# Performance work log

Hardware: AMD Instinct MI355X
Metric: run time of the kernel (lower is better)

## Reference

```python
import jax, jax.numpy as jnp
import numpy as np

NUM_HEADS = 16
HEAD_DIM = 64  # hidden_size / num_heads


def setup_inputs() -> dict:
    key = jax.random.key(0)
    ks = jax.random.split(key, 20)
    B, S, H, K = 16, 1024, 1024, 64
    d = {"hidden_states": jax.random.normal(ks[0], (B, S, H), jnp.float32)}
    i = 1
    for p in ("q", "k", "v", "o"):
        d["W" + p] = jax.random.normal(ks[i], (H, H), jnp.float32) * (1.0 / np.sqrt(H)); i += 1
        d["b" + p] = jax.random.normal(ks[i], (H,), jnp.float32) * 0.02; i += 1
        d["LM" + p] = jax.random.normal(ks[i], (H, K), jnp.float32) * (1.0 / np.sqrt(K)); i += 1
        d["RM" + p] = jax.random.normal(ks[i], (K, H), jnp.float32) * (1.0 / np.sqrt(H)); i += 1
        d["F" + p] = jnp.ones((H,), jnp.float32)
    d["task"] = 0
    return d


def _proj(x, W, b, LM, RM, F):
    # RG weight reconstruction: weight = LM @ RM + W  (task==0 branch)
    w = LM @ RM + W  # [h_out, h_in]
    y = jnp.einsum("bsi,oi->bso", x, w) + b
    return y * F  # SFG per-channel scaling


def reference(hidden_states, Wq, bq, LMq, RMq, Fq, Wk, bk, LMk, RMk, Fk,
              Wv, bv, LMv, RMv, Fv, Wo, bo, LMo, RMo, Fo, task):
    B, S, H = hidden_states.shape
    nh, hd = NUM_HEADS, HEAD_DIM
    q = _proj(hidden_states, Wq, bq, LMq, RMq, Fq).reshape(B, S, nh, hd)
    k = _proj(hidden_states, Wk, bk, LMk, RMk, Fk).reshape(B, S, nh, hd)
    v = _proj(hidden_states, Wv, bv, LMv, RMv, Fv).reshape(B, S, nh, hd)
    scores = jnp.einsum("bqhd,bkhd->bhqk", q, k) / np.sqrt(hd).astype(np.float32)
    probs = jax.nn.softmax(scores, axis=-1)  # attn_dropout rate = 0.0
    ctx = jnp.einsum("bhqk,bkhd->bqhd", probs, v).reshape(B, S, H)
    out = _proj(ctx, Wo, bo, LMo, RMo, Fo)  # proj_dropout rate = 0.0
    return out
```

## Files before the change

### kernel.cpp

```cpp
#include <hip/hip_runtime.h>
#include <cstdint>
#include <cstddef>

typedef short short8 __attribute__((ext_vector_type(8)));
typedef float f32x4 __attribute__((ext_vector_type(4)));
typedef unsigned short us4 __attribute__((ext_vector_type(4)));
typedef unsigned int u32x2 __attribute__((ext_vector_type(2)));

__device__ __forceinline__ unsigned short f2bf(float f) {
  unsigned int u = __float_as_uint(f);
  unsigned int r = (u + 0x7fffu + ((u >> 16) & 1u)) >> 16;
  return (unsigned short)r;
}
__device__ __forceinline__ float exp2_fast(float x) {
  return __builtin_amdgcn_exp2f(x);
}
__device__ __forceinline__ unsigned int cvt_pk_bf16(float a, float b) {
  unsigned int d;
  asm("v_cvt_pk_bf16_f32 %0, %1, %2" : "=v"(d) : "v"(a), "v"(b));
  return d;
}
__device__ __forceinline__ void gload_lds16(const void* g, void* l) {
  auto gp = reinterpret_cast<const __attribute__((address_space(1))) char*>(
      reinterpret_cast<uintptr_t>(g));
  auto lp = reinterpret_cast<__attribute__((address_space(3))) char*>(
      reinterpret_cast<uintptr_t>(l));
  __builtin_amdgcn_global_load_lds(gp, lp, 16, 0, 0);
}

__global__ __launch_bounds__(256) void prep_weights(
    const float* __restrict__ W, const float* __restrict__ bias,
    const float* __restrict__ LM, const float* __restrict__ RM,
    const float* __restrict__ F, float scale,
    unsigned short* __restrict__ Wout, float* __restrict__ bout) {
  const int o = blockIdx.x;
  const int tid = threadIdx.x;
  __shared__ float lm[64];
  if (tid < 64) lm[tid] = LM[o * 64 + tid];
  __syncthreads();
  const float f = F[o] * scale;
#pragma unroll
  for (int j = 0; j < 4; ++j) {
    const int i = tid + j * 256;
    float acc = W[o * 1024 + i];
#pragma unroll 16
    for (int k = 0; k < 64; ++k) acc = fmaf(lm[k], RM[k * 1024 + i], acc);
    Wout[o * 1024 + i] = f2bf(acc * f);
  }
  if (tid == 0) bout[o] = bias[o] * f;
}

__global__ __launch_bounds__(256) void cast_x(const float* __restrict__ x,
                                              unsigned short* __restrict__ y, int n4) {
  const int i = blockIdx.x * 256 + threadIdx.x;
  if (i >= n4) return;
  f32x4 v = *(const f32x4*)(x + (size_t)i * 4);
  us4 o;
  o[0] = f2bf(v[0]); o[1] = f2bf(v[1]); o[2] = f2bf(v[2]); o[3] = f2bf(v[3]);
  *(us4*)(y + (size_t)i * 4) = o;
}

template <int MODE>
__global__ __launch_bounds__(256) void gemm_bt(const unsigned short* __restrict__ A,
                                               const unsigned short* __restrict__ Bw,
                                               const float* __restrict__ bias,
                                               void* __restrict__ Cout,
                                               int M, int N, int K) {
  __shared__ unsigned short sA[128 * 64];
  __shared__ unsigned short sB[128 * 64];
  const int tid = threadIdx.x;
  const int w = tid >> 6;
  const int lane = tid & 63;
  const int quad = lane >> 4;
  const int ln = lane & 15;
  const int bm = blockIdx.x, bn = blockIdx.y;
  const int wm = w >> 1, wn = w & 1;

  f32x4 acc[4][4];
#pragma unroll
  for (int a = 0; a < 4; ++a)
#pragma unroll
    for (int b = 0; b < 4; ++b) acc[a][b] = (f32x4){0.f, 0.f, 0.f, 0.f};

  const size_t Kb = (size_t)K * 2;
  const char* Agb = (const char*)A + (size_t)bm * 128 * Kb;
  const char* Bgb = (const char*)Bw + (size_t)bn * 128 * Kb;
  char* sAb = (char*)sA;
  char* sBb = (char*)sB;
  const int sw = ln & 7;

  for (int k0 = 0; k0 < K; k0 += 64) {
    __syncthreads();
#pragma unroll
    for (int i = 0; i < 4; ++i) {
      const int Lb = w * 4096 + i * 1024 + lane * 16;
      const int r = Lb >> 7;
      const int c = (Lb >> 4) & 7;
      const int cb = ((c ^ (r & 7)) * 16);
      gload_lds16(Agb + (size_t)r * Kb + (size_t)k0 * 2 + cb, sAb + Lb);
      gload_lds16(Bgb + (size_t)r * Kb + (size_t)k0 * 2 + cb, sBb + Lb);
    }
    __syncthreads();
#pragma unroll
    for (int kk = 0; kk < 2; ++kk) {
      short8 af[4], bfv[4];
#pragma unroll
      for (int t = 0; t < 4; ++t) {
        const int ch = ((kk * 4 + quad) ^ sw) * 16;
        af[t]  = *(const short8*)(sAb + (wm * 64 + t * 16 + ln) * 128 + ch);
        bfv[t] = *(const short8*)(sBb + (wn * 64 + t * 16 + ln) * 128 + ch);
      }
#pragma unroll
      for (int mt = 0; mt < 4; ++mt)
#pragma unroll
        for (int nt = 0; nt < 4; ++nt)
          acc[mt][nt] = __builtin_amdgcn_mfma_f32_16x16x32_bf16(af[mt], bfv[nt], acc[mt][nt], 0, 0, 0);
    }
  }

  if (MODE == 0) {
    unsigned short* out = (unsigned short*)Cout;
#pragma unroll
    for (int mt = 0; mt < 4; ++mt) {
#pragma unroll
      for (int nt = 0; nt < 4; ++nt) {
        const int gn = bn * 128 + wn * 64 + nt * 16 + ln;
        const float bv = bias[gn];
        const int pidx = gn >> 10, rem = gn & 1023;
        const int hh = rem >> 6, dd = rem & 63;
        const int gm0 = bm * 128 + wm * 64 + mt * 16 + quad * 4;
        const int bb = gm0 >> 10, ss0 = gm0 & 1023;
        if (pidx < 2) {
#pragma unroll
          for (int r = 0; r < 4; ++r) {
            const size_t off = ((((size_t)pidx * 16 + bb) * 16 + hh) * 1024 + (ss0 + r)) * 64 + dd;
            out[off] = f2bf(acc[mt][nt][r] + bv);
          }
        } else {
          us4 pk;
#pragma unroll
          for (int r = 0; r < 4; ++r) pk[r] = f2bf(acc[mt][nt][r] + bv);
          const size_t off = (size_t)2 * 16777216 +
                             (((size_t)(bb * 16 + hh) * 64 + dd) * 1024 + ss0);
          *(us4*)(out + off) = pk;
        }
      }
    }
  } else {
    float* out = (float*)Cout;
#pragma unroll
    for (int mt = 0; mt < 4; ++mt) {
#pragma unroll
      for (int nt = 0; nt < 4; ++nt) {
        const int gn = bn * 128 + wn * 64 + nt * 16 + ln;
        const float bv = bias[gn];
#pragma unroll
        for (int r = 0; r < 4; ++r) {
          const int gm = bm * 128 + wm * 64 + mt * 16 + quad * 4 + r;
          out[(size_t)gm * N + gn] = acc[mt][nt][r] + bv;
        }
      }
    }
  }
}

__global__ __launch_bounds__(256) void attn(const unsigned short* __restrict__ Qb,
                                            const unsigned short* __restrict__ Kb_,
                                            const unsigned short* __restrict__ VTb,
                                            unsigned short* __restrict__ ctx) {
  __shared__ unsigned short sK[64 * 64];
  __shared__ unsigned short sVT[64 * 64];
  __shared__ unsigned short sP[64 * 72];
  const int tid = threadIdx.x;
  const int w = tid >> 6, lane = tid & 63, quad = lane >> 4, ln = lane & 15;
  const int qt = blockIdx.x, bh = blockIdx.y;
  const int b = bh >> 4, h = bh & 15;

  char* sKb = (char*)sK;
  char* sVb = (char*)sVT;
  char* sPb = (char*)sP;
  const int sw = ln & 7;

  const unsigned short* Qg = Qb + ((size_t)bh * 1024 + (size_t)qt * 64 + w * 16 + ln) * 64;
  const short8 bq0 = *(const short8*)(Qg + quad * 8);
  const short8 bq1 = *(const short8*)(Qg + 32 + quad * 8);

  f32x4 accO[4];
#pragma unroll
  for (int nt = 0; nt < 4; ++nt) accO[nt] = (f32x4){0.f, 0.f, 0.f, 0.f};
  float mrun = -3e38f, lrun = 0.f;

  for (int kt = 0; kt < 16; ++kt) {
    __syncthreads();
    const char* Kg = (const char*)(Kb_ + ((size_t)bh * 1024 + (size_t)kt * 64) * 64);
    const char* Vg = (const char*)(VTb + (size_t)bh * 65536 + (size_t)kt * 64);
#pragma unroll
    for (int i = 0; i < 2; ++i) {
      const int Lb = w * 2048 + i * 1024 + lane * 16;
      const int r = Lb >> 7;
      const int c = (Lb >> 4) & 7;
      const int cb = ((c ^ (r & 7)) * 16);
      gload_lds16(Kg + (size_t)r * 128 + cb, sKb + Lb);
      gload_lds16(Vg + (size_t)r * 2048 + cb, sVb + Lb);
    }
    __syncthreads();

    f32x4 accS[4];
#pragma unroll
    for (int mt = 0; mt < 4; ++mt) accS[mt] = (f32x4){0.f, 0.f, 0.f, 0.f};
#pragma unroll
    for (int mt = 0; mt < 4; ++mt) {
      const short8 ak0 = *(const short8*)(sKb + (mt * 16 + ln) * 128 + (quad ^ sw) * 16);
      accS[mt] = __builtin_amdgcn_mfma_f32_16x16x32_bf16(ak0, bq0, accS[mt], 0, 0, 0);
    }
#pragma unroll
    for (int mt = 0; mt < 4; ++mt) {
      const short8 ak1 = *(const short8*)(sKb + (mt * 16 + ln) * 128 + ((4 + quad) ^ sw) * 16);
      accS[mt] = __builtin_amdgcn_mfma_f32_16x16x32_bf16(ak1, bq1, accS[mt], 0, 0, 0);
    }

    float tmax = -3e38f;
#pragma unroll
    for (int mt = 0; mt < 4; ++mt)
#pragma unroll
      for (int r = 0; r < 4; ++r) tmax = fmaxf(tmax, accS[mt][r]);
    tmax = fmaxf(tmax, __shfl_xor(tmax, 16));
    tmax = fmaxf(tmax, __shfl_xor(tmax, 32));
    const float mnew = fmaxf(mrun, tmax);
    const float alpha = exp2_fast(mrun - mnew);
    mrun = mnew;
    float psum = 0.f;
#pragma unroll
    for (int mt = 0; mt < 4; ++mt) {
      float p0 = exp2_fast(accS[mt][0] - mnew);
      float p1 = exp2_fast(accS[mt][1] - mnew);
      float p2 = exp2_fast(accS[mt][2] - mnew);
      float p3 = exp2_fast(accS[mt][3] - mnew);
      psum += (p0 + p1) + (p2 + p3);
      u32x2 pk;
      pk[0] = cvt_pk_bf16(p0, p1);
      pk[1] = cvt_pk_bf16(p2, p3);
      *(u32x2*)(sP + (w * 16 + ln) * 72 + mt * 16 + quad * 4) = pk;
    }
    psum += __shfl_xor(psum, 16);
    psum += __shfl_xor(psum, 32);
    lrun = lrun * alpha + psum;
#pragma unroll
    for (int r = 0; r < 4; ++r) {
      const float ar = __shfl(alpha, quad * 4 + r);
#pragma unroll
      for (int nt = 0; nt < 4; ++nt) accO[nt][r] *= ar;
    }

#pragma unroll
    for (int kk = 0; kk < 2; ++kk) {
      const short8 ap = *(const short8*)(sPb + (w * 16 + ln) * 144 + kk * 64 + quad * 16);
#pragma unroll
      for (int nt = 0; nt < 4; ++nt) {
        const short8 bv = *(const short8*)(sVb + (nt * 16 + ln) * 128 + ((kk * 4 + quad) ^ sw) * 16);
        accO[nt] = __builtin_amdgcn_mfma_f32_16x16x32_bf16(ap, bv, accO[nt], 0, 0, 0);
      }
    }
  }

  const float inv = 1.0f / lrun;
#pragma unroll
  for (int r = 0; r < 4; ++r) {
    const float ivr = __shfl(inv, quad * 4 + r);
    const int s = qt * 64 + w * 16 + quad * 4 + r;
#pragma unroll
    for (int nt = 0; nt < 4; ++nt) {
      const int d = nt * 16 + ln;
      ctx[((size_t)(b * 1024 + s)) * 1024 + h * 64 + d] = f2bf(accO[nt][r] * ivr);
    }
  }
}

extern "C" void kernel_launch(void* const* d_in, const int* in_sizes, int n_in,
                              void* d_out, int out_size, void* d_ws, size_t ws_size,
                              hipStream_t stream) {
  const float* hs  = (const float*)d_in[0];
  const float* Wq  = (const float*)d_in[1];
  const float* bq  = (const float*)d_in[2];
  const float* LMq = (const float*)d_in[3];
  const float* RMq = (const float*)d_in[4];
  const float* Fq  = (const float*)d_in[5];
  const float* Wk  = (const float*)d_in[6];
  const float* bk  = (const float*)d_in[7];
  const float* LMk = (const float*)d_in[8];
  const float* RMk = (const float*)d_in[9];
  const float* Fk  = (const float*)d_in[10];
  const float* Wv  = (const float*)d_in[11];
  const float* bv  = (const float*)d_in[12];
  const float* LMv = (const float*)d_in[13];
  const float* RMv = (const float*)d_in[14];
  const float* Fv  = (const float*)d_in[15];
  const float* Wo  = (const float*)d_in[16];
  const float* bo  = (const float*)d_in[17];
  const float* LMo = (const float*)d_in[18];
  const float* RMo = (const float*)d_in[19];
  const float* Fo  = (const float*)d_in[20];

  char* p = (char*)d_ws;
  unsigned short* xbf  = (unsigned short*)p; p += (size_t)16384 * 1024 * 2;
  unsigned short* Wqkv = (unsigned short*)p; p += (size_t)3072 * 1024 * 2;
  unsigned short* Wob  = (unsigned short*)p; p += (size_t)1024 * 1024 * 2;
  float* bqkv = (float*)p; p += 3072 * 4;
  float* bob  = (float*)p; p += 1024 * 4;
  unsigned short* qkv = (unsigned short*)p; p += (size_t)3 * 16777216 * 2;
  unsigned short* ctx = (unsigned short*)p; p += (size_t)16777216 * 2;

  const float qscale = 0.125f * 1.4426950408889634f;

  cast_x<<<16384, 256, 0, stream>>>(hs, xbf, 16777216 / 4);
  prep_weights<<<1024, 256, 0, stream>>>(Wq, bq, LMq, RMq, Fq, qscale, Wqkv, bqkv);
  prep_weights<<<1024, 256, 0, stream>>>(Wk, bk, LMk, RMk, Fk, 1.0f, Wqkv + 1024 * 1024, bqkv + 1024);
  prep_weights<<<1024, 256, 0, stream>>>(Wv, bv, LMv, RMv, Fv, 1.0f, Wqkv + 2 * 1024 * 1024, bqkv + 2048);
  prep_weights<<<1024, 256, 0, stream>>>(Wo, bo, LMo, RMo, Fo, 1.0f, Wob, bob);

  gemm_bt<0><<<dim3(128, 24), 256, 0, stream>>>(xbf, Wqkv, bqkv, (void*)qkv, 16384, 3072, 1024);

  attn<<<dim3(16, 256), 256, 0, stream>>>(qkv, qkv + 16777216, qkv + 2 * 16777216, ctx);

  gemm_bt<1><<<dim3(128, 8), 256, 0, stream>>>(ctx, Wob, bob, d_out, 16384, 1024, 1024);
}
```

Before: 522.2 us.

## Process 128 queries per attention block and remap blocks across XCDs

Each wave now handles two 16-row query subtiles, so every K/V tile loaded into shared memory serves 128 queries instead of 64. This halves global K/V traffic and the number of barrier-separated load phases per query, and reuses each K/V fragment read from LDS across two MFMAs. The grid is flattened and block IDs are remapped so that all query tiles of one (batch, head) land on the same XCD, aiming to improve L2 reuse of K/V. The cost is more registers per thread, a larger sP buffer and half as many blocks.

```diff
diff --git a/kernel.cpp b/kernel.cpp
--- a/kernel.cpp
+++ b/kernel.cpp
@@ -5,7 +5,6 @@
 typedef short short8 __attribute__((ext_vector_type(8)));
 typedef float f32x4 __attribute__((ext_vector_type(4)));
 typedef unsigned short us4 __attribute__((ext_vector_type(4)));
-typedef unsigned int u32x2 __attribute__((ext_vector_type(2)));
 
 __device__ __forceinline__ unsigned short f2bf(float f) {
   unsigned int u = __float_as_uint(f);
@@ -170,10 +169,12 @@
                                             unsigned short* __restrict__ ctx) {
   __shared__ unsigned short sK[64 * 64];
   __shared__ unsigned short sVT[64 * 64];
-  __shared__ unsigned short sP[64 * 72];
+  __shared__ unsigned short sP[128 * 72];
   const int tid = threadIdx.x;
   const int w = tid >> 6, lane = tid & 63, quad = lane >> 4, ln = lane & 15;
-  const int qt = blockIdx.x, bh = blockIdx.y;
+  const int bid = blockIdx.x;
+  const int xcd = bid & 7, qt = (bid >> 3) & 7, sbh = bid >> 6;
+  const int bh = xcd * 32 + sbh;
   const int b = bh >> 4, h = bh & 15;
 
   char* sKb = (char*)sK;
@@ -181,14 +182,21 @@
   char* sPb = (char*)sP;
   const int sw = ln & 7;
 
-  const unsigned short* Qg = Qb + ((size_t)bh * 1024 + (size_t)qt * 64 + w * 16 + ln) * 64;
-  const short8 bq0 = *(const short8*)(Qg + quad * 8);
-  const short8 bq1 = *(const short8*)(Qg + 32 + quad * 8);
-
-  f32x4 accO[4];
-#pragma unroll
-  for (int nt = 0; nt < 4; ++nt) accO[nt] = (f32x4){0.f, 0.f, 0.f, 0.f};
-  float mrun = -3e38f, lrun = 0.f;
+  short8 bq[2][2];
+#pragma unroll
+  for (int s = 0; s < 2; ++s) {
+    const unsigned short* Qg =
+        Qb + ((size_t)bh * 1024 + (size_t)qt * 128 + w * 32 + s * 16 + ln) * 64;
+    bq[s][0] = *(const short8*)(Qg + quad * 8);
+    bq[s][1] = *(const short8*)(Qg + 32 + quad * 8);
+  }
+
+  f32x4 accO[2][4];
+#pragma unroll
+  for (int s = 0; s < 2; ++s)
+#pragma unroll
+    for (int nt = 0; nt < 4; ++nt) accO[s][nt] = (f32x4){0.f, 0.f, 0.f, 0.f};
+  float mrun[2] = {-3e38f, -3e38f}, lrun[2] = {0.f, 0.f};
 
   for (int kt = 0; kt < 16; ++kt) {
     __syncthreads();
@@ -205,73 +213,90 @@
     }
     __syncthreads();
 
-    f32x4 accS[4];
-#pragma unroll
-    for (int mt = 0; mt < 4; ++mt) accS[mt] = (f32x4){0.f, 0.f, 0.f, 0.f};
-#pragma unroll
-    for (int mt = 0; mt < 4; ++mt) {
-      const short8 ak0 = *(const short8*)(sKb + (mt * 16 + ln) * 128 + (quad ^ sw) * 16);
-      accS[mt] = __builtin_amdgcn_mfma_f32_16x16x32_bf16(ak0, bq0, accS[mt], 0, 0, 0);
-    }
-#pragma unroll
-    for (int mt = 0; mt < 4; ++mt) {
-      const short8 ak1 = *(const short8*)(sKb + (mt * 16 + ln) * 128 + ((4 + quad) ^ sw) * 16);
-      accS[mt] = __builtin_amdgcn_mfma_f32_16x16x32_bf16(ak1, bq1, accS[mt], 0, 0, 0);
-    }
-
-    float tmax = -3e38f;
-#pragma unroll
-    for (int mt = 0; mt < 4; ++mt)
-#pragma unroll
-      for (int r = 0; r < 4; ++r) tmax = fmaxf(tmax, accS[mt][r]);
-    tmax = fmaxf(tmax, __shfl_xor(tmax, 16));
-    tmax = fmaxf(tmax, __shfl_xor(tmax, 32));
-    const float mnew = fmaxf(mrun, tmax);
-    const float alpha = exp2_fast(mrun - mnew);
-    mrun = mnew;
-    float psum = 0.f;
-#pragma unroll
-    for (int mt = 0; mt < 4; ++mt) {
-      float p0 = exp2_fast(accS[mt][0] - mnew);
-      float p1 = exp2_fast(accS[mt][1] - mnew);
-      float p2 = exp2_fast(accS[mt][2] - mnew);
-      float p3 = exp2_fast(accS[mt][3] - mnew);
-      psum += (p0 + p1) + (p2 + p3);
-      u32x2 pk;
-      pk[0] = cvt_pk_bf16(p0, p1);
-      pk[1] = cvt_pk_bf16(p2, p3);
-      *(u32x2*)(sP + (w * 16 + ln) * 72 + mt * 16 + quad * 4) = pk;
-    }
-    psum += __shfl_xor(psum, 16);
-    psum += __shfl_xor(psum, 32);
-    lrun = lrun * alpha + psum;
-#pragma unroll
-    for (int r = 0; r < 4; ++r) {
-      const float ar = __shfl(alpha, quad * 4 + r);
-#pragma unroll
-      for (int nt = 0; nt < 4; ++nt) accO[nt][r] *= ar;
-    }
-
+    f32x4 accS[2][4];
+#pragma unroll
+    for (int s = 0; s < 2; ++s)
+#pragma unroll
+      for (int mt = 0; mt < 4; ++mt) accS[s][mt] = (f32x4){0.f, 0.f, 0.f, 0.f};
 #pragma unroll
     for (int kk = 0; kk < 2; ++kk) {
-      const short8 ap = *(const short8*)(sPb + (w * 16 + ln) * 144 + kk * 64 + quad * 16);
+      short8 ak[4];
+#pragma unroll
+      for (int mt = 0; mt < 4; ++mt)
+        ak[mt] = *(const short8*)(sKb + (mt * 16 + ln) * 128 + ((kk * 4 + quad) ^ sw) * 16);
+#pragma unroll
+      for (int s = 0; s < 2; ++s)
+#pragma unroll
+        for (int mt = 0; mt < 4; ++mt)
+          accS[s][mt] = __builtin_amdgcn_mfma_f32_16x16x32_bf16(ak[mt], bq[s][kk], accS[s][mt], 0, 0, 0);
+    }
+
+#pragma unroll
+    for (int s = 0; s < 2; ++s) {
+      float tmax = -3e38f;
+#pragma unroll
+      for (int mt = 0; mt < 4; ++mt)
+#pragma unroll
+        for (int r = 0; r < 4; ++r) tmax = fmaxf(tmax, accS[s][mt][r]);
+      tmax = fmaxf(tmax, __shfl_xor(tmax, 16));
+      tmax = fmaxf(tmax, __shfl_xor(tmax, 32));
+      const float mnew = fmaxf(mrun[s], tmax);
+      const float alpha = exp2_fast(mrun[s] - mnew);
+      mrun[s] = mnew;
+      float psum = 0.f;
+#pragma unroll
+      for (int mt = 0; mt < 4; ++mt) {
+        float p0 = exp2_fast(accS[s][mt][0] - mnew);
+        float p1 = exp2_fast(accS[s][mt][1] - mnew);
+        float p2 = exp2_fast(accS[s][mt][2] - mnew);
+        float p3 = exp2_fast(accS[s][mt][3] - mnew);
+        psum += (p0 + p1) + (p2 + p3);
+        union { unsigned int u[2]; us4 v; } pu;
+        pu.u[0] = cvt_pk_bf16(p0, p1);
+        pu.u[1] = cvt_pk_bf16(p2, p3);
+        *(us4*)(sP + (w * 32 + s * 16 + ln) * 72 + mt * 16 + quad * 4) = pu.v;
+      }
+      psum += __shfl_xor(psum, 16);
+      psum += __shfl_xor(psum, 32);
+      lrun[s] = lrun[s] * alpha + psum;
+#pragma unroll
+      for (int r = 0; r < 4; ++r) {
+        const float ar = __shfl(alpha, quad * 4 + r);
+#pragma unroll
+        for (int nt = 0; nt < 4; ++nt) accO[s][nt][r] *= ar;
+      }
+    }
+
+    asm volatile("" ::: "memory");
+
+#pragma unroll
+    for (int kk = 0; kk < 2; ++kk) {
+      short8 ap[2];
+#pragma unroll
+      for (int s = 0; s < 2; ++s)
+        ap[s] = *(const short8*)(sPb + (w * 32 + s * 16 + ln) * 144 + kk * 64 + quad * 16);
 #pragma unroll
       for (int nt = 0; nt < 4; ++nt) {
         const short8 bv = *(const short8*)(sVb + (nt * 16 + ln) * 128 + ((kk * 4 + quad) ^ sw) * 16);
-        accO[nt] = __builtin_amdgcn_mfma_f32_16x16x32_bf16(ap, bv, accO[nt], 0, 0, 0);
-      }
-    }
-  }
-
-  const float inv = 1.0f / lrun;
-#pragma unroll
-  for (int r = 0; r < 4; ++r) {
-    const float ivr = __shfl(inv, quad * 4 + r);
-    const int s = qt * 64 + w * 16 + quad * 4 + r;
-#pragma unroll
-    for (int nt = 0; nt < 4; ++nt) {
-      const int d = nt * 16 + ln;
-      ctx[((size_t)(b * 1024 + s)) * 1024 + h * 64 + d] = f2bf(accO[nt][r] * ivr);
+#pragma unroll
+        for (int s = 0; s < 2; ++s)
+          accO[s][nt] = __builtin_amdgcn_mfma_f32_16x16x32_bf16(ap[s], bv, accO[s][nt], 0, 0, 0);
+      }
+    }
+  }
+
+#pragma unroll
+  for (int s = 0; s < 2; ++s) {
+    const float inv = 1.0f / lrun[s];
+#pragma unroll
+    for (int r = 0; r < 4; ++r) {
+      const float ivr = __shfl(inv, quad * 4 + r);
+      const int sg = qt * 128 + w * 32 + s * 16 + quad * 4 + r;
+#pragma unroll
+      for (int nt = 0; nt < 4; ++nt) {
+        const int d = nt * 16 + ln;
+        ctx[((size_t)(b * 1024 + sg)) * 1024 + h * 64 + d] = f2bf(accO[s][nt][r] * ivr);
+      }
     }
   }
 }
@@ -320,7 +345,7 @@
 
   gemm_bt<0><<<dim3(128, 24), 256, 0, stream>>>(xbf, Wqkv, bqkv, (void*)qkv, 16384, 3072, 1024);
 
-  attn<<<dim3(16, 256), 256, 0, stream>>>(qkv, qkv + 16777216, qkv + 2 * 16777216, ctx);
+  attn<<<2048, 256, 0, stream>>>(qkv, qkv + 16777216, qkv + 2 * 16777216, ctx);
 
   gemm_bt<1><<<dim3(128, 8), 256, 0, stream>>>(ctx, Wob, bob, d_out, 16384, 1024, 1024);
 }
```

New measurement: 514.5 us. Within noise of the previous version (-1.5%).
